# Optimization experiments

Measured on AMD Instinct MI355X. Metric: run time of the kernel, lower is better.

## Reference

```python
import jax, jax.numpy as jnp
import numpy as np
from jax import lax

NUM_SAMPLE = 1024   # init_kwargs: num_sample
RADIUS = 0.1        # init_kwargs: ball_query_radius (compared against SQUARED distance, as in original)


def setup_inputs() -> dict:
    key = jax.random.key(0)
    x = jax.random.normal(key, (4, 32768, 131), dtype=jnp.float32)  # [B, N, 3+C]
    return {"x": x}


def _fps_single(pts, num_sample):
    # pts: [N, 3]. Faithful to source: seed index is overwritten at i=0, so the
    # only effect of the seed is the first distance update; we use a
    # deterministic seed of 0 instead of python random.randint.
    n = pts.shape[0]

    def step(carry, _):
        closest, sel = carry
        d = jnp.sum((pts[sel] - pts) ** 2, axis=-1)      # [N]
        closest = jnp.minimum(d, closest)
        sel = jnp.argmax(closest).astype(jnp.int32)
        return (closest, sel), sel

    init = (jnp.full((n,), jnp.inf, dtype=jnp.float32), jnp.int32(0))
    _, idx = lax.scan(step, init, None, length=num_sample)
    return idx  # [M] int32


def _ball_query_counts(pts, idx, radius):
    # pts: [N,3], idx: [M]. Original builds variable-length index lists; the
    # jit-static equivalent is the membership mask d2 <= radius. We return the
    # per-centroid member counts (summary of the mask).
    cent = pts[idx]                                                 # [M, 3]
    d2 = jnp.sum((cent[:, None, :] - pts[None, :, :]) ** 2, axis=-1)  # [M, N]
    return jnp.sum(d2 <= radius, axis=-1).astype(jnp.int32)          # [M]


def reference(x):
    pts = x[:, :, :3]                                    # [B, N, 3]
    idx = jax.vmap(lambda p: _fps_single(p, NUM_SAMPLE))(pts)            # [B, M]
    counts = jax.vmap(lambda p, i: _ball_query_counts(p, i, RADIUS))(pts, idx)  # [B, M]
    # Original forward returns x unchanged; idx/counts are returned as well so
    # the FPS + ball-query compute is observable and not dead-code-eliminated.
    return (x, idx, counts)
```

## Files before the change

kernel.cpp:

```cpp
#include <hip/hip_runtime.h>
#include <math.h>

#define B 4
#define N 32768
#define D 131
#define S 1024
#define RAD2 0.1f
#define G 8
#define TPB 512
#define PPT 8
#define NFPS (B * G)
#define COPY_BLOCKS 192
#define SLOT_STRIDE 8

__global__ void pack_kernel(const float* __restrict__ x, float* __restrict__ ws) {
    int i = blockIdx.x * blockDim.x + threadIdx.x;
    if (i < B * N) {
        const float* __restrict__ s = x + (size_t)i * D;
        float a = s[0], bb = s[1], c = s[2];
        ws[i]             = a;
        ws[B * N + i]     = bb;
        ws[2 * B * N + i] = c;
        float4* w4 = (float4*)(ws + (size_t)3 * B * N);
        w4[i] = make_float4(a, bb, c, 0.0f);
    }
}

__launch_bounds__(TPB)
__global__ void fps_copy_kernel(const float* __restrict__ x,
                                const float* __restrict__ ws,
                                unsigned long long* __restrict__ gslot,
                                float* __restrict__ out_idx,
                                int* __restrict__ idx_int,
                                float* __restrict__ out_x) {
    if (blockIdx.x >= NFPS) {
        const size_t total4 = (size_t)B * N * D / 4;
        const float4* __restrict__ src = (const float4*)x;
        float4* __restrict__ dst = (float4*)out_x;
        for (size_t i = (size_t)(blockIdx.x - NFPS) * TPB + threadIdx.x; i < total4;
             i += (size_t)COPY_BLOCKS * TPB)
            dst[i] = src[i];
        return;
    }

    const int b = blockIdx.x >> 3;
    const int g = blockIdx.x & 7;
    const int t = threadIdx.x;
    const int lane = t & 63;
    const int w = t >> 6;

    __shared__ float s_x[N / G], s_y[N / G], s_z[N / G];
    __shared__ unsigned long long s_wk[2][8];
    __shared__ float s_bc[3];
    __shared__ unsigned s_tag;

    const float* __restrict__ px = ws + (size_t)b * N;
    const float* __restrict__ py = ws + (size_t)(B + b) * N;
    const float* __restrict__ pz = ws + (size_t)(2 * B + b) * N;
    const float4* __restrict__ p4 = (const float4*)(ws + (size_t)3 * B * N) + (size_t)b * N;
    unsigned long long* __restrict__ slots = gslot + (size_t)b * 2 * G * SLOT_STRIDE;

    const int base = g * (N / G);
    float lcl[PPT];
    #pragma unroll
    for (int i = 0; i < PPT / 2; ++i) {
        const int l = 2 * t + 2 * TPB * i;
        *(float2*)&s_x[l] = *(const float2*)&px[base + l];
        *(float2*)&s_y[l] = *(const float2*)&py[base + l];
        *(float2*)&s_z[l] = *(const float2*)&pz[base + l];
        lcl[2*i] = INFINITY; lcl[2*i+1] = INFINITY;
    }
    if (t == 0) s_tag = 0;
    __syncthreads();

    float4 cq = p4[0];
    float cx = cq.x, cy = cq.y, cz = cq.z;

    for (int s = 0; s < S; ++s) {
        float best = -INFINITY;
        int   bidx = 0;
        #pragma unroll
        for (int i = 0; i < PPT / 2; ++i) {
            const int l = 2 * t + 2 * TPB * i;
            float2 vx = *(const float2*)&s_x[l];
            float2 vy = *(const float2*)&s_y[l];
            float2 vz = *(const float2*)&s_z[l];
            {
                float dx = __fsub_rn(cx, vx.x);
                float dy = __fsub_rn(cy, vy.x);
                float dz = __fsub_rn(cz, vz.x);
                float d2 = __fadd_rn(__fadd_rn(__fmul_rn(dx, dx), __fmul_rn(dy, dy)),
                                     __fmul_rn(dz, dz));
                float c = fminf(lcl[2*i], d2);
                lcl[2*i] = c;
                if (c > best) { best = c; bidx = base + l; }
            }
            {
                float dx = __fsub_rn(cx, vx.y);
                float dy = __fsub_rn(cy, vy.y);
                float dz = __fsub_rn(cz, vz.y);
                float d2 = __fadd_rn(__fadd_rn(__fmul_rn(dx, dx), __fmul_rn(dy, dy)),
                                     __fmul_rn(dz, dz));
                float c = fminf(lcl[2*i+1], d2);
                lcl[2*i+1] = c;
                if (c > best) { best = c; bidx = base + l + 1; }
            }
        }

        unsigned hi  = __float_as_uint(best);
        unsigned lo2 = (unsigned)(32767 - bidx);
        #define FPS_COMBINE(OHI, OLO) \
            { unsigned _oh = (OHI), _ol = (OLO); \
              if (_oh > hi || (_oh == hi && _ol > lo2)) { hi = _oh; lo2 = _ol; } }
        { unsigned a = (unsigned)__builtin_amdgcn_update_dpp(0, (int)hi, 0xB1, 0xf, 0xf, true);
          unsigned c2 = (unsigned)__builtin_amdgcn_update_dpp(0, (int)lo2, 0xB1, 0xf, 0xf, true);
          FPS_COMBINE(a, c2); }
        { unsigned a = (unsigned)__builtin_amdgcn_update_dpp(0, (int)hi, 0x4E, 0xf, 0xf, true);
          unsigned c2 = (unsigned)__builtin_amdgcn_update_dpp(0, (int)lo2, 0x4E, 0xf, 0xf, true);
          FPS_COMBINE(a, c2); }
        { unsigned a = (unsigned)__builtin_amdgcn_update_dpp(0, (int)hi, 0x141, 0xf, 0xf, true);
          unsigned c2 = (unsigned)__builtin_amdgcn_update_dpp(0, (int)lo2, 0x141, 0xf, 0xf, true);
          FPS_COMBINE(a, c2); }
        { unsigned a = (unsigned)__builtin_amdgcn_update_dpp(0, (int)hi, 0x140, 0xf, 0xf, true);
          unsigned c2 = (unsigned)__builtin_amdgcn_update_dpp(0, (int)lo2, 0x140, 0xf, 0xf, true);
          FPS_COMBINE(a, c2); }
        { unsigned a = (unsigned)__builtin_amdgcn_ds_swizzle((int)hi, 0x401F);
          unsigned c2 = (unsigned)__builtin_amdgcn_ds_swizzle((int)lo2, 0x401F);
          FPS_COMBINE(a, c2); }
        { unsigned a = (unsigned)__shfl_xor((int)hi, 32, 64);
          unsigned c2 = (unsigned)__shfl_xor((int)lo2, 32, 64);
          FPS_COMBINE(a, c2); }
        #undef FPS_COMBINE

        const int buf = s & 1;
        const unsigned tag = (unsigned)(s + 1);
        const unsigned long long mykey = ((unsigned long long)hi << 32) |
                                         ((unsigned long long)lo2 << 17) | tag;
        if (lane == 0) s_wk[buf][w] = mykey;
        __syncthreads();

        if (w == 0) {
            unsigned long long bk = s_wk[buf][0];
            #pragma unroll
            for (int j = 1; j < 8; ++j) { unsigned long long v = s_wk[buf][j]; if (v > bk) bk = v; }
            if (lane == 0)
                __hip_atomic_store(&slots[((size_t)buf * G + g) * SLOT_STRIDE], bk,
                                   __ATOMIC_RELAXED, __HIP_MEMORY_SCOPE_AGENT);

            unsigned long long* myslot =
                &slots[((size_t)buf * G + (lane & 7)) * SLOT_STRIDE];
            #define POLL() __hip_atomic_load(myslot, __ATOMIC_RELAXED, __HIP_MEMORY_SCOPE_AGENT)
            unsigned long long q0, q1, q2, q3, kko;
            q0 = POLL(); __builtin_amdgcn_s_sleep(2);
            q1 = POLL(); __builtin_amdgcn_s_sleep(2);
            q2 = POLL(); __builtin_amdgcn_s_sleep(2);
            q3 = POLL();
            for (;;) {
                if (!__any((unsigned)(q0 & 0x7FFull) != tag)) { kko = q0; break; }
                q0 = POLL();
                if (!__any((unsigned)(q1 & 0x7FFull) != tag)) { kko = q1; break; }
                q1 = POLL();
                if (!__any((unsigned)(q2 & 0x7FFull) != tag)) { kko = q2; break; }
                q2 = POLL();
                if (!__any((unsigned)(q3 & 0x7FFull) != tag)) { kko = q3; break; }
                q3 = POLL();
            }
            #undef POLL

            const int idxc = 32767 - (int)((kko >> 17) & 0x7FFF);
            const float4 cand = p4[idxc];

            unsigned long long kk = kko;
            #pragma unroll
            for (int off = 1; off < 8; off <<= 1) {
                unsigned long long o = (unsigned long long)__shfl_xor((long long)kk, off, 64);
                if (o > kk) kk = o;
            }
            unsigned long long mask = __ballot(kko == kk);
            int src = (int)(__ffsll((unsigned long long)mask) - 1);
            cx = __shfl(cand.x, src, 64);
            cy = __shfl(cand.y, src, 64);
            cz = __shfl(cand.z, src, 64);

            if (lane == 0) {
                s_bc[0] = cx; s_bc[1] = cy; s_bc[2] = cz;
                __threadfence_block();
                __hip_atomic_store(&s_tag, tag, __ATOMIC_RELAXED,
                                   __HIP_MEMORY_SCOPE_WORKGROUP);
                if (g == 0) {
                    int sel = 32767 - (int)((kk >> 17) & 0x7FFF);
                    out_idx[(size_t)b * S + s] = (float)sel;
                    idx_int[b * S + s] = sel;
                }
            }
        } else {
            while (__hip_atomic_load(&s_tag, __ATOMIC_RELAXED,
                                     __HIP_MEMORY_SCOPE_WORKGROUP) != tag) {}
            __threadfence_block();
            cx = s_bc[0]; cy = s_bc[1]; cz = s_bc[2];
        }
    }
}

__launch_bounds__(256)
__global__ void ballq_kernel(const float* __restrict__ ws,
                             const int* __restrict__ idx_int,
                             float* __restrict__ out_counts) {
    __shared__ int s_part[4];
    const int b = blockIdx.x >> 10;
    const int j = blockIdx.x & 1023;
    const int t = threadIdx.x;
    const float* __restrict__ px = ws + (size_t)b * N;
    const float* __restrict__ py = ws + (size_t)(B + b) * N;
    const float* __restrict__ pz = ws + (size_t)(2 * B + b) * N;

    const int ci = idx_int[b * S + j];
    const float cx = px[ci], cy = py[ci], cz = pz[ci];

    int cnt = 0;
    #pragma unroll 4
    for (int p = t; p < N; p += 256) {
        float dx = __fsub_rn(cx, px[p]);
        float dy = __fsub_rn(cy, py[p]);
        float dz = __fsub_rn(cz, pz[p]);
        float d2 = __fadd_rn(__fadd_rn(__fmul_rn(dx, dx), __fmul_rn(dy, dy)),
                             __fmul_rn(dz, dz));
        cnt += (d2 <= RAD2) ? 1 : 0;
    }
    #pragma unroll
    for (int off = 1; off < 64; off <<= 1)
        cnt += __shfl_xor(cnt, off, 64);
    if ((t & 63) == 0) s_part[t >> 6] = cnt;
    __syncthreads();
    if (t == 0)
        out_counts[b * S + j] = (float)(s_part[0] + s_part[1] + s_part[2] + s_part[3]);
}

extern "C" void kernel_launch(void* const* d_in, const int* in_sizes, int n_in,
                              void* d_out, int out_size, void* d_ws, size_t ws_size,
                              hipStream_t stream) {
    const float* x = (const float*)d_in[0];
    float* out = (float*)d_out;
    float* ws = (float*)d_ws;
    int* idx_int = (int*)(ws + (size_t)7 * B * N);
    unsigned long long* gslot = (unsigned long long*)(idx_int + B * S);

    float* out_x      = out;
    float* out_idx    = out + (size_t)B * N * D;
    float* out_counts = out_idx + (size_t)B * S;

    hipMemsetAsync(gslot, 0,
                   (size_t)B * 2 * G * SLOT_STRIDE * sizeof(unsigned long long), stream);

    hipLaunchKernelGGL(pack_kernel, dim3((B * N + 255) / 256), dim3(256), 0, stream, x, ws);
    hipLaunchKernelGGL(fps_copy_kernel, dim3(NFPS + COPY_BLOCKS), dim3(TPB), 0, stream,
                       x, ws, gslot, out_idx, idx_int, out_x);
    hipLaunchKernelGGL(ballq_kernel, dim3(B * S), dim3(256), 0, stream, ws, idx_int, out_counts);
}
```

Baseline: 2.298 ms.

## Co-locate each batch's FPS blocks on one XCD with fewer, larger blocks

Cuts the FPS group from 8 blocks of 512 threads to 4 blocks of 1024 threads per batch. Block ids are remapped so that all of a batch's FPS blocks share the same bid&7 value, which under round-robin dispatch should place them on the same XCD and let the cross-block slot exchange stay in a shared L2. The spin-wait now uses sc0 global loads with an occasional agent-scope atomic load. The in-block wave reduction becomes a shuffle tree over 16 waves. The aim is lower per-step cross-block synchronization latency across the 1024 serial FPS steps, at the cost of more points per block and a smaller copy grid.

```diff
diff --git a/kernel.cpp b/kernel.cpp
--- a/kernel.cpp
+++ b/kernel.cpp
@@ -6,12 +6,13 @@
 #define D 131
 #define S 1024
 #define RAD2 0.1f
-#define G 8
-#define TPB 512
+#define G 4
+#define TPB 1024
 #define PPT 8
-#define NFPS (B * G)
-#define COPY_BLOCKS 192
+#define SLICE (N / G)
 #define SLOT_STRIDE 8
+#define NB_TOTAL 128
+#define COPY_BLOCKS 112
 
 __global__ void pack_kernel(const float* __restrict__ x, float* __restrict__ ws) {
     int i = blockIdx.x * blockDim.x + threadIdx.x;
@@ -26,6 +27,14 @@
     }
 }
 
+__device__ inline unsigned long long ld_sc0(const unsigned long long* p) {
+    unsigned long long v;
+    asm volatile("global_load_dwordx2 %0, %1, off sc0\n\t"
+                 "s_waitcnt vmcnt(0)"
+                 : "=v"(v) : "v"(p) : "memory");
+    return v;
+}
+
 __launch_bounds__(TPB)
 __global__ void fps_copy_kernel(const float* __restrict__ x,
                                 const float* __restrict__ ws,
@@ -33,24 +42,29 @@
                                 float* __restrict__ out_idx,
                                 int* __restrict__ idx_int,
                                 float* __restrict__ out_x) {
-    if (blockIdx.x >= NFPS) {
+    const int bid = blockIdx.x;
+    const bool is_fps = (bid < 32) && ((bid & 7) < 4);
+
+    if (!is_fps) {
+        int ci = (bid >= 32) ? (16 + (bid - 32))
+                             : ((bid >> 3) * 4 + ((bid & 7) - 4));
         const size_t total4 = (size_t)B * N * D / 4;
         const float4* __restrict__ src = (const float4*)x;
         float4* __restrict__ dst = (float4*)out_x;
-        for (size_t i = (size_t)(blockIdx.x - NFPS) * TPB + threadIdx.x; i < total4;
+        for (size_t i = (size_t)ci * TPB + threadIdx.x; i < total4;
              i += (size_t)COPY_BLOCKS * TPB)
             dst[i] = src[i];
         return;
     }
 
-    const int b = blockIdx.x >> 3;
-    const int g = blockIdx.x & 7;
+    const int b = bid & 7;
+    const int g = bid >> 3;
     const int t = threadIdx.x;
     const int lane = t & 63;
     const int w = t >> 6;
 
-    __shared__ float s_x[N / G], s_y[N / G], s_z[N / G];
-    __shared__ unsigned long long s_wk[2][8];
+    __shared__ float s_x[SLICE], s_y[SLICE], s_z[SLICE];
+    __shared__ unsigned long long s_wk[2][16];
     __shared__ float s_bc[3];
     __shared__ unsigned s_tag;
 
@@ -60,7 +74,7 @@
     const float4* __restrict__ p4 = (const float4*)(ws + (size_t)3 * B * N) + (size_t)b * N;
     unsigned long long* __restrict__ slots = gslot + (size_t)b * 2 * G * SLOT_STRIDE;
 
-    const int base = g * (N / G);
+    const int base = g * SLICE;
     float lcl[PPT];
     #pragma unroll
     for (int i = 0; i < PPT / 2; ++i) {
@@ -140,39 +154,36 @@
         __syncthreads();
 
         if (w == 0) {
-            unsigned long long bk = s_wk[buf][0];
+            unsigned long long bk = s_wk[buf][lane & 15];
             #pragma unroll
-            for (int j = 1; j < 8; ++j) { unsigned long long v = s_wk[buf][j]; if (v > bk) bk = v; }
-            if (lane == 0)
-                __hip_atomic_store(&slots[((size_t)buf * G + g) * SLOT_STRIDE], bk,
-                                   __ATOMIC_RELAXED, __HIP_MEMORY_SCOPE_AGENT);
-
-            unsigned long long* myslot =
-                &slots[((size_t)buf * G + (lane & 7)) * SLOT_STRIDE];
-            #define POLL() __hip_atomic_load(myslot, __ATOMIC_RELAXED, __HIP_MEMORY_SCOPE_AGENT)
-            unsigned long long q0, q1, q2, q3, kko;
-            q0 = POLL(); __builtin_amdgcn_s_sleep(2);
-            q1 = POLL(); __builtin_amdgcn_s_sleep(2);
-            q2 = POLL(); __builtin_amdgcn_s_sleep(2);
-            q3 = POLL();
+            for (int off = 1; off < 16; off <<= 1) {
+                unsigned long long o = (unsigned long long)__shfl_xor((long long)bk, off, 64);
+                if (o > bk) bk = o;
+            }
+            unsigned long long* wslot = &slots[((size_t)buf * G + g) * SLOT_STRIDE];
+            if (lane == 0) {
+                asm volatile("global_store_dwordx2 %0, %1, off"
+                             :: "v"(wslot), "v"(bk) : "memory");
+                __hip_atomic_store(wslot, bk, __ATOMIC_RELAXED,
+                                   __HIP_MEMORY_SCOPE_AGENT);
+            }
+
+            unsigned long long* myslot = &slots[((size_t)buf * G + (lane & 3)) * SLOT_STRIDE];
+            unsigned long long kko;
+            int it = 0;
             for (;;) {
-                if (!__any((unsigned)(q0 & 0x7FFull) != tag)) { kko = q0; break; }
-                q0 = POLL();
-                if (!__any((unsigned)(q1 & 0x7FFull) != tag)) { kko = q1; break; }
-                q1 = POLL();
-                if (!__any((unsigned)(q2 & 0x7FFull) != tag)) { kko = q2; break; }
-                q2 = POLL();
-                if (!__any((unsigned)(q3 & 0x7FFull) != tag)) { kko = q3; break; }
-                q3 = POLL();
-            }
-            #undef POLL
+                kko = (++it & 7) ? ld_sc0(myslot)
+                                 : __hip_atomic_load(myslot, __ATOMIC_RELAXED,
+                                                     __HIP_MEMORY_SCOPE_AGENT);
+                if (!__any((unsigned)(kko & 0x7FFull) != tag)) break;
+            }
 
             const int idxc = 32767 - (int)((kko >> 17) & 0x7FFF);
             const float4 cand = p4[idxc];
 
             unsigned long long kk = kko;
             #pragma unroll
-            for (int off = 1; off < 8; off <<= 1) {
+            for (int off = 1; off < 4; off <<= 1) {
                 unsigned long long o = (unsigned long long)__shfl_xor((long long)kk, off, 64);
                 if (o > kk) kk = o;
             }
@@ -253,7 +264,7 @@
                    (size_t)B * 2 * G * SLOT_STRIDE * sizeof(unsigned long long), stream);
 
     hipLaunchKernelGGL(pack_kernel, dim3((B * N + 255) / 256), dim3(256), 0, stream, x, ws);
-    hipLaunchKernelGGL(fps_copy_kernel, dim3(NFPS + COPY_BLOCKS), dim3(TPB), 0, stream,
+    hipLaunchKernelGGL(fps_copy_kernel, dim3(NB_TOTAL), dim3(TPB), 0, stream,
                        x, ws, gslot, out_idx, idx_int, out_x);
     hipLaunchKernelGGL(ballq_kernel, dim3(B * S), dim3(256), 0, stream, ws, idx_int, out_counts);
 }
```

New measurement: 2.940 ms. 1.28x slower.
